# Performance work log

Hardware: AMD Instinct MI355X
Metric: run time of the kernel (lower is better)

Reference implementation:

```python
import jax, jax.numpy as jnp
import numpy as np

N = 50000      # num_nodes
E = 400000     # num_edges
ND = 128       # node_dim (== hidden_dim of GraphNetwork)
HID = 128      # per-head hidden dim in GAT layer
HEADS = 4      # GAT default num_heads
L = 3          # num_layers


def setup_inputs() -> dict:
    key = jax.random.key(0)
    ks = jax.random.split(key, 12)
    s = lambda k, shape, fan: (jax.random.normal(k, shape, jnp.float32) / np.sqrt(fan)).astype(jnp.float32)
    return dict(
        node_features=jax.random.normal(ks[0], (N, ND), jnp.float32),
        edge_index=jax.random.randint(ks[1], (2, E), 0, N, dtype=jnp.int32),
        enc_w1=s(ks[2], (ND, HID), ND), enc_b1=jnp.zeros((HID,), jnp.float32),
        enc_w2=s(ks[3], (HID, HID), HID), enc_b2=jnp.zeros((HID,), jnp.float32),
        gat_W=s(ks[4], (L, HID, HEADS * HID), HID),
        gat_a_src=s(ks[5], (L, HEADS, HID), HID),
        gat_a_dst=s(ks[6], (L, HEADS, HID), HID),
        gat_out_w=s(ks[7], (L, HEADS * HID, HID), HEADS * HID),
        gat_out_b=jnp.zeros((L, HID), jnp.float32),
        out_w1=s(ks[8], (HID, HID), HID), out_b1=jnp.zeros((HID,), jnp.float32),
        out_w2=s(ks[9], (HID, HID), HID), out_b2=jnp.zeros((HID,), jnp.float32),
    )


def _gat_layer(x, row, col, W, a_src, a_dst, ow, ob):
    """One GraphAttentionLayer (eval mode: dropout disabled)."""
    n = x.shape[0]
    h = (x @ W).reshape(n, HEADS, HID)                       # [N,H,D]
    # per-node attention logits (equivalent to (h[row]*a_src).sum(-1) gathered)
    s_src = jnp.einsum('nhd,hd->nh', h, a_src)               # [N,H]
    s_dst = jnp.einsum('nhd,hd->nh', h, a_dst)               # [N,H]
    e = s_src[row] + s_dst[col]                              # [E,H]
    e = jnp.where(e > 0, e, 0.2 * e)                         # LeakyReLU(0.2)
    e_exp = jnp.exp(e)                                       # matches torch: raw exp, no max-shift
    e_sum = jax.ops.segment_sum(e_exp, col, num_segments=n)  # [N,H]
    alpha = e_exp / (e_sum[col] + 1e-8)                      # [E,H]
    msg = h[row] * alpha[:, :, None]                         # [E,H,D]
    out = jax.ops.segment_sum(msg, col, num_segments=n)      # [N,H,D]
    out = out.reshape(n, HEADS * HID) @ ow + ob              # out_proj
    return x + out                                           # residual


def reference(node_features, edge_index, enc_w1, enc_b1, enc_w2, enc_b2,
              gat_W, gat_a_src, gat_a_dst, gat_out_w, gat_out_b,
              out_w1, out_b1, out_w2, out_b2):
    row, col = edge_index[0], edge_index[1]
    # node encoder: Linear-ReLU-Linear
    h = jax.nn.relu(node_features @ enc_w1 + enc_b1) @ enc_w2 + enc_b2
    for i in range(L):
        h = _gat_layer(h, row, col, gat_W[i], gat_a_src[i], gat_a_dst[i],
                       gat_out_w[i], gat_out_b[i])
    # output MLP: Linear-ReLU-Linear
    h = jax.nn.relu(h @ out_w1 + out_b1) @ out_w2 + out_b2
    # batch is None, global_pooling='mean'
    graph_embedding = h.mean(axis=0, keepdims=True)          # [1,HID]
    return h, graph_embedding
```

## Files before the change

### kernel.cpp

```cpp
#include <hip/hip_runtime.h>
#include <math.h>

typedef unsigned short ushort_t;
typedef __attribute__((ext_vector_type(8))) unsigned short ushortx8;
typedef __attribute__((ext_vector_type(4))) unsigned short ushortx4;
typedef __attribute__((ext_vector_type(4))) float floatx4;
typedef __attribute__((ext_vector_type(8))) short frag8;

__device__ __forceinline__ float bf2f(ushort_t u){
  union {unsigned int i; float f;} v; v.i = ((unsigned int)u)<<16; return v.f;
}
__device__ __forceinline__ ushort_t f2bf(float f){
  union {float f; unsigned int i;} v; v.f = f;
  unsigned int x = v.i;
  unsigned int r = x + 0x7fffu + ((x>>16)&1u);
  return (ushort_t)(r>>16);
}

__device__ __forceinline__ void gload16(const void* g, void* l){
  __builtin_amdgcn_global_load_lds(
      (const __attribute__((address_space(1))) unsigned int*)g,
      (__attribute__((address_space(3))) unsigned int*)l, 16, 0, 0);
}

__global__ __launch_bounds__(256) void k_count(const int* __restrict__ col, int* __restrict__ cnt, int E){
  int e = blockIdx.x*256 + threadIdx.x;
  if (e < E) atomicAdd(&cnt[col[e]], 1);
}

__global__ __launch_bounds__(256) void k_scan1(const int* __restrict__ cnt, int* __restrict__ offs,
                                               int* __restrict__ partials, int n){
  __shared__ int buf[256];
  int tid = threadIdx.x;
  int gid = blockIdx.x*256 + tid;
  int v = (gid < n) ? cnt[gid] : 0;
  buf[tid] = v; __syncthreads();
  #pragma unroll
  for (int off=1; off<256; off<<=1){
    int t = (tid >= off) ? buf[tid-off] : 0;
    __syncthreads();
    buf[tid] += t;
    __syncthreads();
  }
  if (gid < n) offs[gid] = buf[tid] - v;
  if (tid == 255) partials[blockIdx.x] = buf[255];
}

__global__ __launch_bounds__(256) void k_scan2(int* __restrict__ partials, int nb){
  __shared__ int buf[256];
  int tid = threadIdx.x;
  int v = (tid < nb) ? partials[tid] : 0;
  buf[tid] = v; __syncthreads();
  #pragma unroll
  for (int off=1; off<256; off<<=1){
    int t = (tid >= off) ? buf[tid-off] : 0;
    __syncthreads();
    buf[tid] += t;
    __syncthreads();
  }
  partials[tid] = buf[tid] - v;
}

__global__ __launch_bounds__(256) void k_scan3(int* __restrict__ offs, const int* __restrict__ partials,
                                               int n, int E){
  int gid = blockIdx.x*256 + threadIdx.x;
  if (gid < n) offs[gid] += partials[blockIdx.x];
  if (blockIdx.x == 0 && threadIdx.x == 0) offs[n] = E;
}

__global__ __launch_bounds__(256) void k_fill(const int* __restrict__ row, const int* __restrict__ col,
                                              const int* __restrict__ offs, int* __restrict__ fill,
                                              int* __restrict__ rowS, int E){
  int e = blockIdx.x*256 + threadIdx.x;
  if (e >= E) return;
  int c = col[e];
  int pos = offs[c] + atomicAdd(&fill[c], 1);
  rowS[pos] = row[e];
}

__global__ __launch_bounds__(256) void k_conv4(const float* __restrict__ src, ushort_t* __restrict__ dst, int n4){
  int i = blockIdx.x*256 + threadIdx.x;
  if (i >= n4) return;
  floatx4 v = ((const floatx4*)src)[i];
  ushortx4 o;
  #pragma unroll
  for (int j=0;j<4;j++) o[j] = f2bf(v[j]);
  ((ushortx4*)dst)[i] = o;
}

template<int K, int NC, int CNT>
__global__ __launch_bounds__(256) void k_convT_b(const float* __restrict__ src, ushort_t* __restrict__ dst){
  int idx = blockIdx.x*256 + threadIdx.x;
  if (idx >= CNT*K*NC) return;
  int l = idx / (K*NC);
  int rem = idx - l*(K*NC);
  int k = rem / NC, n = rem - k*NC;
  dst[(size_t)l*K*NC + (size_t)n*K + k] = f2bf(src[idx]);
}

__global__ __launch_bounds__(256) void k_convT4(const float* __restrict__ s0, const float* __restrict__ s1,
                                                const float* __restrict__ s2, const float* __restrict__ s3,
                                                ushort_t* __restrict__ d0, ushort_t* __restrict__ d1,
                                                ushort_t* __restrict__ d2, ushort_t* __restrict__ d3){
  int idx = blockIdx.x*256 + threadIdx.x;
  if (idx >= 4*16384) return;
  int which = idx >> 14;
  int rem = idx & 16383;
  int k = rem >> 7, n = rem & 127;
  const float* s = which==0 ? s0 : which==1 ? s1 : which==2 ? s2 : s3;
  ushort_t*    d = which==0 ? d0 : which==1 ? d1 : which==2 ? d2 : d3;
  d[n*128 + k] = f2bf(s[rem]);
}

template<bool RELU, bool BIAS, bool RESID, int OMODE, bool SDST, bool COLSUM>
__global__ __launch_bounds__(256) void mfma_gemm(
    const ushort_t* __restrict__ A, const ushort_t* __restrict__ BT,
    const float* __restrict__ bias, const float* __restrict__ resid,
    float* __restrict__ Cf, ushort_t* __restrict__ Cb,
    const float* __restrict__ avec_s, const float* __restrict__ avec_d,
    float* __restrict__ s_src, float* __restrict__ s_dst,
    float* __restrict__ colpart,
    int M, int K, int NC)
{
  __shared__ ushort_t As[128*64];
  __shared__ ushort_t Bs[128*64];
  const int tid  = threadIdx.x;
  const int wid  = tid >> 6, lane = tid & 63;
  const int bm   = blockIdx.y * 128, bn = blockIdx.x * 128;
  const int wr   = (wid >> 1) * 64, wc = (wid & 1) * 64;
  const int lm   = lane & 15;
  const int lk   = (lane >> 4) * 8;

  floatx4 acc[4][4];
  #pragma unroll
  for (int i=0;i<4;i++)
    #pragma unroll
    for (int j=0;j<4;j++) acc[i][j] = floatx4{0.f,0.f,0.f,0.f};

  for (int kc = 0; kc < K; kc += 64){
    #pragma unroll
    for (int i = 0; i < 4; i++){
      int chunk = wid*256 + i*64 + lane;
      int r  = chunk >> 3;
      int c8 = chunk & 7;
      int gr = bm + r; if (gr >= M) gr = M - 1;
      gload16(A  + (size_t)gr*K + kc + c8*8, (char*)As + (size_t)chunk*16);
      gload16(BT + (size_t)(bn + r)*K + kc + c8*8, (char*)Bs + (size_t)chunk*16);
    }
    __syncthreads();

    #pragma unroll
    for (int ks = 0; ks < 2; ks++){
      frag8 a[4], b[4];
      #pragma unroll
      for (int mi=0;mi<4;mi++)
        a[mi] = *(const frag8*)&As[(wr + mi*16 + lm)*64 + ks*32 + lk];
      #pragma unroll
      for (int ni=0;ni<4;ni++)
        b[ni] = *(const frag8*)&Bs[(wc + ni*16 + lm)*64 + ks*32 + lk];
      #pragma unroll
      for (int mi=0;mi<4;mi++)
        #pragma unroll
        for (int ni=0;ni<4;ni++)
          acc[mi][ni] = __builtin_amdgcn_mfma_f32_16x16x32_bf16(a[mi], b[ni], acc[mi][ni], 0, 0, 0);
    }
    __syncthreads();
  }

  const int lr4 = (lane >> 4) * 4;

  float csum[4];
  #pragma unroll
  for (int i=0;i<4;i++) csum[i] = 0.f;

  #pragma unroll
  for (int mi=0;mi<4;mi++){
    #pragma unroll
    for (int ni=0;ni<4;ni++){
      int colg = bn + wc + ni*16 + lm;
      #pragma unroll
      for (int r=0;r<4;r++){
        int rowg = bm + wr + mi*16 + lr4 + r;
        if (rowg < M){
          float v = acc[mi][ni][r];
          if (BIAS)  v += bias[colg];
          if (RELU)  v = v > 0.f ? v : 0.f;
          if (RESID) v += resid[(size_t)rowg*NC + colg];
          if (OMODE == 0 || OMODE == 2) Cf[(size_t)rowg*NC + colg] = v;
          if (OMODE == 1 || OMODE == 2) Cb[(size_t)rowg*NC + colg] = f2bf(v);
          if (COLSUM) csum[ni] += v;
        }
      }
    }
  }

  if constexpr (COLSUM){
    float* sred = (float*)As;
    #pragma unroll
    for (int ni=0;ni<4;ni++){
      float cs = csum[ni];
      cs += __shfl_xor(cs, 16);
      cs += __shfl_xor(cs, 32);
      if (lane < 16)
        sred[(wid>>1)*128 + wc + ni*16 + lane] = cs;
    }
    __syncthreads();
    if (tid < 128)
      colpart[(size_t)blockIdx.y*128 + tid] = sred[tid] + sred[128 + tid];
  }

  if constexpr (SDST){
    const int head = blockIdx.x;
    float* sred = (float*)As;
    float avs[4], avd[4];
    #pragma unroll
    for (int ni=0;ni<4;ni++){
      int d = wc + ni*16 + lm;
      avs[ni] = avec_s[head*128 + d];
      avd[ni] = avec_d[head*128 + d];
    }
    float pss[4][4], psd[4][4];
    #pragma unroll
    for (int mi=0;mi<4;mi++){
      #pragma unroll
      for (int r=0;r<4;r++){
        float vs = 0.f, vd = 0.f;
        #pragma unroll
        for (int ni=0;ni<4;ni++){
          float v = acc[mi][ni][r];
          vs += v * avs[ni];
          vd += v * avd[ni];
        }
        #pragma unroll
        for (int m=1;m<16;m<<=1){
          vs += __shfl_xor(vs, m);
          vd += __shfl_xor(vd, m);
        }
        pss[mi][r] = vs; psd[mi][r] = vd;
      }
    }
    if (lm == 0){
      #pragma unroll
      for (int mi=0;mi<4;mi++)
        #pragma unroll
        for (int r=0;r<4;r++){
          int rl = wr + mi*16 + lr4 + r;
          sred[0*256 + (wid&1)*128 + rl] = pss[mi][r];
          sred[1*256 + (wid&1)*128 + rl] = psd[mi][r];
        }
    }
    __syncthreads();
    int sd = tid >> 7, rl = tid & 127;
    float v = sred[sd*256 + rl] + sred[sd*256 + 128 + rl];
    int rowg = bm + rl;
    if (rowg < M){
      (sd ? s_dst : s_src)[(size_t)rowg*4 + head] = v;
    }
  }
}

__global__ __launch_bounds__(256) void k_gather(const ushort_t* __restrict__ h,
    const float* __restrict__ s_src, const float* __restrict__ s_dst,
    const int* __restrict__ offs, const int* __restrict__ rowS,
    ushort_t* __restrict__ msg, int N)
{
  int wid = threadIdx.x >> 6, lane = threadIdx.x & 63;
  int n = blockIdx.x*4 + wid;
  if (n >= N) return;
  int beg = offs[n], end = offs[n+1];
  const int sub  = lane & 15;
  const int head = lane >> 4;
  const float sdv = s_dst[(size_t)n*4 + head];
  const int c0 = lane*8;

  float acc[8];
  #pragma unroll
  for (int k=0;k<8;k++) acc[k] = 0.f;
  float dsum = 0.f;

  for (int chunk = beg; chunk < end; chunk += 16){
    int m = end - chunk; if (m > 16) m = 16;
    int q = chunk + (sub < m ? sub : m-1);
    int r_p = rowS[q];
    float ss = s_src[(size_t)r_p*4 + head];
    float e = ss + sdv;
    e = e > 0.f ? e : 0.2f*e;
    float w = __expf(e);
    if (sub >= m) w = 0.f;
    dsum += w;

    int j = 0;
    for (; j+1 < m; j += 2){
      int r0 = __shfl(r_p, j);
      int r1 = __shfl(r_p, j+1);
      float w0 = __shfl(w, head*16 + j);
      float w1 = __shfl(w, head*16 + j+1);
      ushortx8 h0 = *(const ushortx8*)(h + (size_t)r0*512 + c0);
      ushortx8 h1 = *(const ushortx8*)(h + (size_t)r1*512 + c0);
      #pragma unroll
      for (int k=0;k<8;k++) acc[k] += w0 * bf2f(h0[k]);
      #pragma unroll
      for (int k=0;k<8;k++) acc[k] += w1 * bf2f(h1[k]);
    }
    if (j < m){
      int r0 = __shfl(r_p, j);
      float w0 = __shfl(w, head*16 + j);
      ushortx8 h0 = *(const ushortx8*)(h + (size_t)r0*512 + c0);
      #pragma unroll
      for (int k=0;k<8;k++) acc[k] += w0 * bf2f(h0[k]);
    }
  }

  float d = dsum;
  #pragma unroll
  for (int mask=1; mask<16; mask<<=1) d += __shfl_xor(d, mask);
  float invd = 1.0f / (d + 1e-8f);

  ushortx8 o;
  #pragma unroll
  for (int k=0;k<8;k++) o[k] = f2bf(acc[k]*invd);
  *(ushortx8*)(msg + (size_t)n*512 + c0) = o;
}

__global__ __launch_bounds__(256) void k_csum2(const float* __restrict__ part, float* __restrict__ out,
                                               int nb, int N){
  __shared__ float buf[256];
  int c = threadIdx.x & 127, half = threadIdx.x >> 7;
  float s = 0.f;
  for (int b = half; b < nb; b += 2) s += part[(size_t)b*128 + c];
  buf[threadIdx.x] = s; __syncthreads();
  if (threadIdx.x < 128) out[c] = (buf[c] + buf[128 + c]) / (float)N;
}

extern "C" void kernel_launch(void* const* d_in, const int* in_sizes, int n_in,
                              void* d_out, int out_size, void* d_ws, size_t ws_size,
                              hipStream_t stream)
{
  const int N = in_sizes[0] / 128;
  const int E = in_sizes[1] / 2;

  const float* nodef  = (const float*)d_in[0];
  const int*   row    = (const int*)d_in[1];
  const int*   col    = row + E;
  const float* enc_w1 = (const float*)d_in[2];
  const float* enc_b1 = (const float*)d_in[3];
  const float* enc_w2 = (const float*)d_in[4];
  const float* enc_b2 = (const float*)d_in[5];
  const float* gat_W  = (const float*)d_in[6];
  const float* a_src  = (const float*)d_in[7];
  const float* a_dst  = (const float*)d_in[8];
  const float* out_w  = (const float*)d_in[9];
  const float* out_b  = (const float*)d_in[10];
  const float* w1     = (const float*)d_in[11];
  const float* b1     = (const float*)d_in[12];
  const float* w2     = (const float*)d_in[13];
  const float* b2     = (const float*)d_in[14];

  char* p = (char*)d_ws;
  auto alloc = [&](size_t bytes)->char*{
    char* r = p; p += (bytes + 255) & ~(size_t)255; return r;
  };
  float*    x     = (float*)   alloc((size_t)N*128*4);
  char*     msgb  =            alloc((size_t)N*512*2);
  ushort_t* h     = (ushort_t*)alloc((size_t)N*512*2);
  ushort_t* xb    = (ushort_t*)alloc((size_t)N*128*2);
  float*    s_src = (float*)   alloc((size_t)N*4*4);
  float*    s_dst = (float*)   alloc((size_t)N*4*4);
  int*      offs  = (int*)     alloc(((size_t)N+1)*4);
  int*      rowS  = (int*)     alloc((size_t)E*4);
  int*      cnt   = (int*)     alloc((size_t)N*4);
  int*      fill  = (int*)     alloc((size_t)N*4);
  int*      parts = (int*)     alloc(1024);
  float*    cpart = (float*)   alloc((size_t)((N+127)/128)*128*4);
  ushort_t* wt_e1 = (ushort_t*)alloc(16384*2);
  ushort_t* wt_e2 = (ushort_t*)alloc(16384*2);
  ushort_t* wt_W  = (ushort_t*)alloc((size_t)3*65536*2);
  ushort_t* wt_o  = (ushort_t*)alloc((size_t)3*65536*2);
  ushort_t* wt_m1 = (ushort_t*)alloc(16384*2);
  ushort_t* wt_m2 = (ushort_t*)alloc(16384*2);

  ushort_t* nfb = h;
  ushort_t* t1  = (ushort_t*)msgb;
  ushort_t* msg = (ushort_t*)msgb;

  hipMemsetAsync(cnt, 0, (size_t)N*4, stream);
  hipMemsetAsync(fill, 0, (size_t)N*4, stream);

  const int gE = (E + 255)/256;
  const int gN = (N + 255)/256;
  const int gW = (N + 3)/4;
  const int gy = (N + 127)/128;
  dim3 blk(256);

  k_count<<<gE, blk, 0, stream>>>(col, cnt, E);
  k_scan1<<<gN, blk, 0, stream>>>(cnt, offs, parts, N);
  k_scan2<<<1,  blk, 0, stream>>>(parts, gN);
  k_scan3<<<gN, blk, 0, stream>>>(offs, parts, N, E);
  k_fill <<<gE, blk, 0, stream>>>(row, col, offs, fill, rowS, E);

  k_convT4<<<(4*16384+255)/256, blk, 0, stream>>>(enc_w1, enc_w2, w1, w2, wt_e1, wt_e2, wt_m1, wt_m2);
  k_convT_b<128,512,3><<<(3*65536+255)/256, blk, 0, stream>>>(gat_W, wt_W);
  k_convT_b<512,128,3><<<(3*65536+255)/256, blk, 0, stream>>>(out_w, wt_o);

  k_conv4<<<(N*128/4 + 255)/256, blk, 0, stream>>>(nodef, nfb, N*128/4);

  mfma_gemm<true ,true ,false,1,false,false><<<dim3(1,gy), blk, 0, stream>>>(nfb, wt_e1, enc_b1, nullptr, nullptr, t1, nullptr, nullptr, nullptr, nullptr, nullptr, N, 128, 128);
  mfma_gemm<false,true ,false,2,false,false><<<dim3(1,gy), blk, 0, stream>>>(t1,  wt_e2, enc_b2, nullptr, x, xb, nullptr, nullptr, nullptr, nullptr, nullptr, N, 128, 128);

  for (int l = 0; l < 3; l++){
    const ushort_t* WT  = wt_W + (size_t)l*65536;
    const ushort_t* OT  = wt_o + (size_t)l*65536;
    const float*    asl = a_src + (size_t)l*512;
    const float*    adl = a_dst + (size_t)l*512;
    const float*    obl = out_b + (size_t)l*128;

    mfma_gemm<false,false,false,1,true,false><<<dim3(4,gy), blk, 0, stream>>>(xb, WT, nullptr, nullptr, nullptr, h, asl, adl, s_src, s_dst, nullptr, N, 128, 512);
    k_gather<<<gW, blk, 0, stream>>>(h, s_src, s_dst, offs, rowS, msg, N);
    mfma_gemm<false,true ,true ,2,false,false><<<dim3(1,gy), blk, 0, stream>>>(msg, OT, obl, x, x, xb, nullptr, nullptr, nullptr, nullptr, nullptr, N, 512, 128);
  }

  mfma_gemm<true ,true ,false,1,false,false><<<dim3(1,gy), blk, 0, stream>>>(xb, wt_m1, b1, nullptr, nullptr, t1, nullptr, nullptr, nullptr, nullptr, nullptr, N, 128, 128);
  mfma_gemm<false,true ,false,0,false,true ><<<dim3(1,gy), blk, 0, stream>>>(t1, wt_m2, b2, nullptr, (float*)d_out, nullptr, nullptr, nullptr, nullptr, nullptr, cpart, N, 128, 128);
  k_csum2<<<1, blk, 0, stream>>>(cpart, (float*)d_out + (size_t)N*128, gy, N);
}
```

Measured before the change: 594.4 us.

## Fuse GEMM chains per row block into encoder, mid-layer and tail kernels

Replaces the separate generic GEMM launches with three fused kernels that keep a 128-row tile in LDS across consecutive GEMMs. The encoder MLP plus the first layer's head projection, each out-projection plus residual plus the next layer's head projection, and the last out-projection plus output MLP plus column sums now each run in one kernel. This removes the bf16 intermediate round trips (t1, xb) and the separate input conversion kernel, and cuts launch count. In exchange the grid for the head projection shrinks from 4×gy to gy blocks, LDS use grows to about 64KB per block, which lowers occupancy, and the four head GEMMs run serially within each block.

Measured after the change: 538.6 us. -9.4%, faster.

```diff
diff --git a/kernel.cpp b/kernel.cpp
--- a/kernel.cpp
+++ b/kernel.cpp
@@ -76,16 +76,6 @@
   int c = col[e];
   int pos = offs[c] + atomicAdd(&fill[c], 1);
   rowS[pos] = row[e];
-}
-
-__global__ __launch_bounds__(256) void k_conv4(const float* __restrict__ src, ushort_t* __restrict__ dst, int n4){
-  int i = blockIdx.x*256 + threadIdx.x;
-  if (i >= n4) return;
-  floatx4 v = ((const floatx4*)src)[i];
-  ushortx4 o;
-  #pragma unroll
-  for (int j=0;j<4;j++) o[j] = f2bf(v[j]);
-  ((ushortx4*)dst)[i] = o;
 }
 
 template<int K, int NC, int CNT>
@@ -112,151 +102,329 @@
   d[n*128 + k] = f2bf(s[rem]);
 }
 
-template<bool RELU, bool BIAS, bool RESID, int OMODE, bool SDST, bool COLSUM>
-__global__ __launch_bounds__(256) void mfma_gemm(
-    const ushort_t* __restrict__ A, const ushort_t* __restrict__ BT,
-    const float* __restrict__ bias, const float* __restrict__ resid,
-    float* __restrict__ Cf, ushort_t* __restrict__ Cb,
-    const float* __restrict__ avec_s, const float* __restrict__ avec_d,
-    float* __restrict__ s_src, float* __restrict__ s_dst,
-    float* __restrict__ colpart,
-    int M, int K, int NC)
+__device__ __forceinline__ void stage_tile64(const ushort_t* src, int ld, int row0, int M, int kc,
+                                             ushort_t* lds, int tid){
+  int wid = tid>>6, lane = tid&63;
+  #pragma unroll
+  for (int i=0;i<4;i++){
+    int chunk = wid*256 + i*64 + lane;
+    int r = chunk>>3, c8 = chunk&7;
+    int gr = row0 + r; if (gr >= M) gr = M-1;
+    gload16(src + (size_t)gr*ld + kc + c8*8, (char*)lds + (size_t)chunk*16);
+  }
+}
+__device__ __forceinline__ void stage_w128(const ushort_t* src, ushort_t* lds, int tid){
+  #pragma unroll
+  for (int i=0;i<8;i++){
+    int chunk = tid + 256*i;
+    gload16(src + (size_t)chunk*8, (char*)lds + (size_t)chunk*16);
+  }
+}
+
+template<int SA,int SB,int NKS>
+__device__ __forceinline__ void ldsgemm(const ushort_t* LA, const ushort_t* LB,
+                                        floatx4 (&acc)[4][4], int wr,int wc,int lm,int lk){
+  #pragma unroll
+  for (int ks=0; ks<NKS; ks++){
+    frag8 a[4], b[4];
+    #pragma unroll
+    for (int mi=0;mi<4;mi++) a[mi] = *(const frag8*)&LA[(wr+mi*16+lm)*SA + ks*32 + lk];
+    #pragma unroll
+    for (int ni=0;ni<4;ni++) b[ni] = *(const frag8*)&LB[(wc+ni*16+lm)*SB + ks*32 + lk];
+    #pragma unroll
+    for (int mi=0;mi<4;mi++)
+      #pragma unroll
+      for (int ni=0;ni<4;ni++)
+        acc[mi][ni] = __builtin_amdgcn_mfma_f32_16x16x32_bf16(a[mi], b[ni], acc[mi][ni], 0, 0, 0);
+  }
+}
+
+__device__ __forceinline__ void zero_acc(floatx4 (&acc)[4][4]){
+  #pragma unroll
+  for (int i=0;i<4;i++)
+    #pragma unroll
+    for (int j=0;j<4;j++) acc[i][j] = floatx4{0.f,0.f,0.f,0.f};
+}
+
+__device__ __forceinline__ void sdst_block(const floatx4 (&acc)[4][4],
+    const float* avec_s, const float* avec_d, float* s_src, float* s_dst, float* sred,
+    int head, int bm, int M, int tid, int wid, int lane, int wr, int wc, int lm, int lr4){
+  float avs[4], avd[4];
+  #pragma unroll
+  for (int ni=0;ni<4;ni++){
+    int d = wc + ni*16 + lm;
+    avs[ni] = avec_s[head*128 + d];
+    avd[ni] = avec_d[head*128 + d];
+  }
+  float pss[4][4], psd[4][4];
+  #pragma unroll
+  for (int mi=0;mi<4;mi++){
+    #pragma unroll
+    for (int r=0;r<4;r++){
+      float vs = 0.f, vd = 0.f;
+      #pragma unroll
+      for (int ni=0;ni<4;ni++){
+        float v = acc[mi][ni][r];
+        vs += v * avs[ni];
+        vd += v * avd[ni];
+      }
+      #pragma unroll
+      for (int m=1;m<16;m<<=1){
+        vs += __shfl_xor(vs, m);
+        vd += __shfl_xor(vd, m);
+      }
+      pss[mi][r] = vs; psd[mi][r] = vd;
+    }
+  }
+  if (lm == 0){
+    #pragma unroll
+    for (int mi=0;mi<4;mi++)
+      #pragma unroll
+      for (int r=0;r<4;r++){
+        int rl = wr + mi*16 + lr4 + r;
+        sred[0*256 + (wid&1)*128 + rl] = pss[mi][r];
+        sred[1*256 + (wid&1)*128 + rl] = psd[mi][r];
+      }
+  }
+  __syncthreads();
+  int sd = tid >> 7, rl = tid & 127;
+  float v = sred[sd*256 + rl] + sred[sd*256 + 128 + rl];
+  int rowg = bm + rl;
+  if (rowg < M) (sd ? s_dst : s_src)[(size_t)rowg*4 + head] = v;
+}
+
+__device__ __forceinline__ void wgemm_heads(const ushort_t* LA_xb, ushort_t* LB,
+    const ushort_t* WT, const float* avs, const float* avd,
+    ushort_t* h, float* s_src, float* s_dst, float* sred,
+    int bm, int M, int tid, int wid, int lane, int wr, int wc, int lm, int lk, int lr4){
+  for (int hb=0; hb<4; hb++){
+    __syncthreads();
+    stage_w128(WT + (size_t)hb*16384, LB, tid);
+    __syncthreads();
+    floatx4 acc[4][4]; zero_acc(acc);
+    ldsgemm<128,128,4>(LA_xb, LB, acc, wr, wc, lm, lk);
+    #pragma unroll
+    for (int mi=0;mi<4;mi++){
+      #pragma unroll
+      for (int ni=0;ni<4;ni++){
+        int colg = wc + ni*16 + lm;
+        #pragma unroll
+        for (int r=0;r<4;r++){
+          int rowg = bm + wr + mi*16 + lr4 + r;
+          if (rowg < M) h[(size_t)rowg*512 + hb*128 + colg] = f2bf(acc[mi][ni][r]);
+        }
+      }
+    }
+    sdst_block(acc, avs, avd, s_src, s_dst, sred, hb, bm, M, tid, wid, lane, wr, wc, lm, lr4);
+  }
+}
+
+__global__ __launch_bounds__(256) void k_enc(
+    const float* __restrict__ nodef,
+    const ushort_t* __restrict__ e1T, const float* __restrict__ eb1,
+    const ushort_t* __restrict__ e2T, const float* __restrict__ eb2,
+    const ushort_t* __restrict__ WT, const float* __restrict__ avs, const float* __restrict__ avd,
+    float* __restrict__ x, ushort_t* __restrict__ h,
+    float* __restrict__ s_src, float* __restrict__ s_dst, int M)
 {
-  __shared__ ushort_t As[128*64];
-  __shared__ ushort_t Bs[128*64];
-  const int tid  = threadIdx.x;
-  const int wid  = tid >> 6, lane = tid & 63;
-  const int bm   = blockIdx.y * 128, bn = blockIdx.x * 128;
-  const int wr   = (wid >> 1) * 64, wc = (wid & 1) * 64;
-  const int lm   = lane & 15;
-  const int lk   = (lane >> 4) * 8;
-
-  floatx4 acc[4][4];
-  #pragma unroll
-  for (int i=0;i<4;i++)
-    #pragma unroll
-    for (int j=0;j<4;j++) acc[i][j] = floatx4{0.f,0.f,0.f,0.f};
-
-  for (int kc = 0; kc < K; kc += 64){
-    #pragma unroll
-    for (int i = 0; i < 4; i++){
-      int chunk = wid*256 + i*64 + lane;
-      int r  = chunk >> 3;
-      int c8 = chunk & 7;
-      int gr = bm + r; if (gr >= M) gr = M - 1;
-      gload16(A  + (size_t)gr*K + kc + c8*8, (char*)As + (size_t)chunk*16);
-      gload16(BT + (size_t)(bn + r)*K + kc + c8*8, (char*)Bs + (size_t)chunk*16);
-    }
-    __syncthreads();
-
-    #pragma unroll
-    for (int ks = 0; ks < 2; ks++){
-      frag8 a[4], b[4];
-      #pragma unroll
-      for (int mi=0;mi<4;mi++)
-        a[mi] = *(const frag8*)&As[(wr + mi*16 + lm)*64 + ks*32 + lk];
-      #pragma unroll
-      for (int ni=0;ni<4;ni++)
-        b[ni] = *(const frag8*)&Bs[(wc + ni*16 + lm)*64 + ks*32 + lk];
-      #pragma unroll
-      for (int mi=0;mi<4;mi++)
-        #pragma unroll
-        for (int ni=0;ni<4;ni++)
-          acc[mi][ni] = __builtin_amdgcn_mfma_f32_16x16x32_bf16(a[mi], b[ni], acc[mi][ni], 0, 0, 0);
-    }
-    __syncthreads();
-  }
-
-  const int lr4 = (lane >> 4) * 4;
+  __shared__ ushort_t LA[128*128];
+  __shared__ ushort_t LB[128*128];
+  __shared__ float sred[512];
+  const int tid = threadIdx.x, wid = tid>>6, lane = tid&63;
+  const int bm = blockIdx.x*128;
+  const int wr = (wid>>1)*64, wc = (wid&1)*64, lm = lane&15, lk = (lane>>4)*8, lr4 = (lane>>4)*4;
+
+  #pragma unroll
+  for (int i=0;i<8;i++){
+    int chunk = tid + 256*i;
+    int r = chunk>>4, c8 = chunk&15;
+    int gr = bm + r; if (gr >= M) gr = M-1;
+    floatx4 lo = *(const floatx4*)(nodef + (size_t)gr*128 + c8*8);
+    floatx4 hi = *(const floatx4*)(nodef + (size_t)gr*128 + c8*8 + 4);
+    ushortx8 v;
+    #pragma unroll
+    for (int j=0;j<4;j++){ v[j] = f2bf(lo[j]); v[j+4] = f2bf(hi[j]); }
+    *(ushortx8*)&LA[r*128 + c8*8] = v;
+  }
+  stage_w128(e1T, LB, tid);
+  __syncthreads();
+
+  floatx4 acc[4][4]; zero_acc(acc);
+  ldsgemm<128,128,4>(LA, LB, acc, wr, wc, lm, lk);
+  __syncthreads();
+  #pragma unroll
+  for (int mi=0;mi<4;mi++)
+    #pragma unroll
+    for (int ni=0;ni<4;ni++){
+      int cl = wc + ni*16 + lm;
+      float b = eb1[cl];
+      #pragma unroll
+      for (int r=0;r<4;r++){
+        float v = acc[mi][ni][r] + b;
+        v = v > 0.f ? v : 0.f;
+        LA[(wr + mi*16 + lr4 + r)*128 + cl] = f2bf(v);
+      }
+    }
+  stage_w128(e2T, LB, tid);
+  __syncthreads();
+
+  zero_acc(acc);
+  ldsgemm<128,128,4>(LA, LB, acc, wr, wc, lm, lk);
+  __syncthreads();
+  #pragma unroll
+  for (int mi=0;mi<4;mi++)
+    #pragma unroll
+    for (int ni=0;ni<4;ni++){
+      int cl = wc + ni*16 + lm;
+      float b = eb2[cl];
+      #pragma unroll
+      for (int r=0;r<4;r++){
+        int rl = wr + mi*16 + lr4 + r;
+        int rowg = bm + rl;
+        float v = acc[mi][ni][r] + b;
+        if (rowg < M) x[(size_t)rowg*128 + cl] = v;
+        LA[rl*128 + cl] = f2bf(v);
+      }
+    }
+
+  wgemm_heads(LA, LB, WT, avs, avd, h, s_src, s_dst, sred,
+              bm, M, tid, wid, lane, wr, wc, lm, lk, lr4);
+}
+
+__global__ __launch_bounds__(256) void k_mid(
+    const ushort_t* __restrict__ msg, const ushort_t* __restrict__ OT, const float* __restrict__ ob,
+    const ushort_t* __restrict__ WT, const float* __restrict__ avs, const float* __restrict__ avd,
+    float* __restrict__ x, ushort_t* __restrict__ h,
+    float* __restrict__ s_src, float* __restrict__ s_dst, int M)
+{
+  __shared__ ushort_t LA[128*128];
+  __shared__ ushort_t LB[128*128];
+  __shared__ float sred[512];
+  const int tid = threadIdx.x, wid = tid>>6, lane = tid&63;
+  const int bm = blockIdx.x*128;
+  const int wr = (wid>>1)*64, wc = (wid&1)*64, lm = lane&15, lk = (lane>>4)*8, lr4 = (lane>>4)*4;
+
+  floatx4 acc[4][4]; zero_acc(acc);
+  for (int kc = 0; kc < 512; kc += 64){
+    stage_tile64(msg, 512, bm, M, kc, LA, tid);
+    stage_tile64(OT,  512, 0, 128, kc, LB, tid);
+    __syncthreads();
+    ldsgemm<64,64,2>(LA, LB, acc, wr, wc, lm, lk);
+    __syncthreads();
+  }
+  #pragma unroll
+  for (int mi=0;mi<4;mi++)
+    #pragma unroll
+    for (int ni=0;ni<4;ni++){
+      int cl = wc + ni*16 + lm;
+      float b = ob[cl];
+      #pragma unroll
+      for (int r=0;r<4;r++){
+        int rl = wr + mi*16 + lr4 + r;
+        int rowg = bm + rl;
+        float v = acc[mi][ni][r] + b;
+        if (rowg < M){
+          v += x[(size_t)rowg*128 + cl];
+          x[(size_t)rowg*128 + cl] = v;
+        }
+        LA[rl*128 + cl] = f2bf(v);
+      }
+    }
+
+  wgemm_heads(LA, LB, WT, avs, avd, h, s_src, s_dst, sred,
+              bm, M, tid, wid, lane, wr, wc, lm, lk, lr4);
+}
+
+__global__ __launch_bounds__(256) void k_tail(
+    const ushort_t* __restrict__ msg, const ushort_t* __restrict__ OT, const float* __restrict__ ob,
+    const ushort_t* __restrict__ m1T, const float* __restrict__ mb1,
+    const ushort_t* __restrict__ m2T, const float* __restrict__ mb2,
+    const float* __restrict__ x, float* __restrict__ out, float* __restrict__ cpart, int M)
+{
+  __shared__ ushort_t LA[128*128];
+  __shared__ ushort_t LB[128*128];
+  __shared__ float sredc[256];
+  const int tid = threadIdx.x, wid = tid>>6, lane = tid&63;
+  const int bm = blockIdx.x*128;
+  const int wr = (wid>>1)*64, wc = (wid&1)*64, lm = lane&15, lk = (lane>>4)*8, lr4 = (lane>>4)*4;
+
+  floatx4 acc[4][4]; zero_acc(acc);
+  for (int kc = 0; kc < 512; kc += 64){
+    stage_tile64(msg, 512, bm, M, kc, LA, tid);
+    stage_tile64(OT,  512, 0, 128, kc, LB, tid);
+    __syncthreads();
+    ldsgemm<64,64,2>(LA, LB, acc, wr, wc, lm, lk);
+    __syncthreads();
+  }
+  #pragma unroll
+  for (int mi=0;mi<4;mi++)
+    #pragma unroll
+    for (int ni=0;ni<4;ni++){
+      int cl = wc + ni*16 + lm;
+      float b = ob[cl];
+      #pragma unroll
+      for (int r=0;r<4;r++){
+        int rl = wr + mi*16 + lr4 + r;
+        int rowg = bm + rl;
+        float v = acc[mi][ni][r] + b;
+        if (rowg < M) v += x[(size_t)rowg*128 + cl];
+        LA[rl*128 + cl] = f2bf(v);
+      }
+    }
+  stage_w128(m1T, LB, tid);
+  __syncthreads();
+
+  zero_acc(acc);
+  ldsgemm<128,128,4>(LA, LB, acc, wr, wc, lm, lk);
+  __syncthreads();
+  #pragma unroll
+  for (int mi=0;mi<4;mi++)
+    #pragma unroll
+    for (int ni=0;ni<4;ni++){
+      int cl = wc + ni*16 + lm;
+      float b = mb1[cl];
+      #pragma unroll
+      for (int r=0;r<4;r++){
+        float v = acc[mi][ni][r] + b;
+        v = v > 0.f ? v : 0.f;
+        LA[(wr + mi*16 + lr4 + r)*128 + cl] = f2bf(v);
+      }
+    }
+  stage_w128(m2T, LB, tid);
+  __syncthreads();
+
+  zero_acc(acc);
+  ldsgemm<128,128,4>(LA, LB, acc, wr, wc, lm, lk);
 
   float csum[4];
   #pragma unroll
   for (int i=0;i<4;i++) csum[i] = 0.f;
-
-  #pragma unroll
-  for (int mi=0;mi<4;mi++){
+  #pragma unroll
+  for (int mi=0;mi<4;mi++)
     #pragma unroll
     for (int ni=0;ni<4;ni++){
-      int colg = bn + wc + ni*16 + lm;
+      int cl = wc + ni*16 + lm;
+      float b = mb2[cl];
       #pragma unroll
       for (int r=0;r<4;r++){
         int rowg = bm + wr + mi*16 + lr4 + r;
         if (rowg < M){
-          float v = acc[mi][ni][r];
-          if (BIAS)  v += bias[colg];
-          if (RELU)  v = v > 0.f ? v : 0.f;
-          if (RESID) v += resid[(size_t)rowg*NC + colg];
-          if (OMODE == 0 || OMODE == 2) Cf[(size_t)rowg*NC + colg] = v;
-          if (OMODE == 1 || OMODE == 2) Cb[(size_t)rowg*NC + colg] = f2bf(v);
-          if (COLSUM) csum[ni] += v;
+          float v = acc[mi][ni][r] + b;
+          out[(size_t)rowg*128 + cl] = v;
+          csum[ni] += v;
         }
       }
     }
-  }
-
-  if constexpr (COLSUM){
-    float* sred = (float*)As;
-    #pragma unroll
-    for (int ni=0;ni<4;ni++){
-      float cs = csum[ni];
-      cs += __shfl_xor(cs, 16);
-      cs += __shfl_xor(cs, 32);
-      if (lane < 16)
-        sred[(wid>>1)*128 + wc + ni*16 + lane] = cs;
-    }
-    __syncthreads();
-    if (tid < 128)
-      colpart[(size_t)blockIdx.y*128 + tid] = sred[tid] + sred[128 + tid];
-  }
-
-  if constexpr (SDST){
-    const int head = blockIdx.x;
-    float* sred = (float*)As;
-    float avs[4], avd[4];
-    #pragma unroll
-    for (int ni=0;ni<4;ni++){
-      int d = wc + ni*16 + lm;
-      avs[ni] = avec_s[head*128 + d];
-      avd[ni] = avec_d[head*128 + d];
-    }
-    float pss[4][4], psd[4][4];
-    #pragma unroll
-    for (int mi=0;mi<4;mi++){
-      #pragma unroll
-      for (int r=0;r<4;r++){
-        float vs = 0.f, vd = 0.f;
-        #pragma unroll
-        for (int ni=0;ni<4;ni++){
-          float v = acc[mi][ni][r];
-          vs += v * avs[ni];
-          vd += v * avd[ni];
-        }
-        #pragma unroll
-        for (int m=1;m<16;m<<=1){
-          vs += __shfl_xor(vs, m);
-          vd += __shfl_xor(vd, m);
-        }
-        pss[mi][r] = vs; psd[mi][r] = vd;
-      }
-    }
-    if (lm == 0){
-      #pragma unroll
-      for (int mi=0;mi<4;mi++)
-        #pragma unroll
-        for (int r=0;r<4;r++){
-          int rl = wr + mi*16 + lr4 + r;
-          sred[0*256 + (wid&1)*128 + rl] = pss[mi][r];
-          sred[1*256 + (wid&1)*128 + rl] = psd[mi][r];
-        }
-    }
-    __syncthreads();
-    int sd = tid >> 7, rl = tid & 127;
-    float v = sred[sd*256 + rl] + sred[sd*256 + 128 + rl];
-    int rowg = bm + rl;
-    if (rowg < M){
-      (sd ? s_dst : s_src)[(size_t)rowg*4 + head] = v;
-    }
-  }
+  __syncthreads();
+  #pragma unroll
+  for (int ni=0;ni<4;ni++){
+    float cs = csum[ni];
+    cs += __shfl_xor(cs, 16);
+    cs += __shfl_xor(cs, 32);
+    if (lane < 16) sredc[(wid>>1)*128 + wc + ni*16 + lane] = cs;
+  }
+  __syncthreads();
+  if (tid < 128) cpart[(size_t)blockIdx.x*128 + tid] = sredc[tid] + sredc[128 + tid];
 }
 
 __global__ __launch_bounds__(256) void k_gather(const ushort_t* __restrict__ h,
@@ -361,9 +529,8 @@
     char* r = p; p += (bytes + 255) & ~(size_t)255; return r;
   };
   float*    x     = (float*)   alloc((size_t)N*128*4);
-  char*     msgb  =            alloc((size_t)N*512*2);
+  ushort_t* msg   = (ushort_t*)alloc((size_t)N*512*2);
   ushort_t* h     = (ushort_t*)alloc((size_t)N*512*2);
-  ushort_t* xb    = (ushort_t*)alloc((size_t)N*128*2);
   float*    s_src = (float*)   alloc((size_t)N*4*4);
   float*    s_dst = (float*)   alloc((size_t)N*4*4);
   int*      offs  = (int*)     alloc(((size_t)N+1)*4);
@@ -379,10 +546,6 @@
   ushort_t* wt_m1 = (ushort_t*)alloc(16384*2);
   ushort_t* wt_m2 = (ushort_t*)alloc(16384*2);
 
-  ushort_t* nfb = h;
-  ushort_t* t1  = (ushort_t*)msgb;
-  ushort_t* msg = (ushort_t*)msgb;
-
   hipMemsetAsync(cnt, 0, (size_t)N*4, stream);
   hipMemsetAsync(fill, 0, (size_t)N*4, stream);
 
@@ -402,24 +565,21 @@
   k_convT_b<128,512,3><<<(3*65536+255)/256, blk, 0, stream>>>(gat_W, wt_W);
   k_convT_b<512,128,3><<<(3*65536+255)/256, blk, 0, stream>>>(out_w, wt_o);
 
-  k_conv4<<<(N*128/4 + 255)/256, blk, 0, stream>>>(nodef, nfb, N*128/4);
-
-  mfma_gemm<true ,true ,false,1,false,false><<<dim3(1,gy), blk, 0, stream>>>(nfb, wt_e1, enc_b1, nullptr, nullptr, t1, nullptr, nullptr, nullptr, nullptr, nullptr, N, 128, 128);
-  mfma_gemm<false,true ,false,2,false,false><<<dim3(1,gy), blk, 0, stream>>>(t1,  wt_e2, enc_b2, nullptr, x, xb, nullptr, nullptr, nullptr, nullptr, nullptr, N, 128, 128);
+  k_enc<<<gy, blk, 0, stream>>>(nodef, wt_e1, enc_b1, wt_e2, enc_b2,
+                                wt_W, a_src, a_dst, x, h, s_src, s_dst, N);
 
   for (int l = 0; l < 3; l++){
-    const ushort_t* WT  = wt_W + (size_t)l*65536;
-    const ushort_t* OT  = wt_o + (size_t)l*65536;
-    const float*    asl = a_src + (size_t)l*512;
-    const float*    adl = a_dst + (size_t)l*512;
-    const float*    obl = out_b + (size_t)l*128;
-
-    mfma_gemm<false,false,false,1,true,false><<<dim3(4,gy), blk, 0, stream>>>(xb, WT, nullptr, nullptr, nullptr, h, asl, adl, s_src, s_dst, nullptr, N, 128, 512);
     k_gather<<<gW, blk, 0, stream>>>(h, s_src, s_dst, offs, rowS, msg, N);
-    mfma_gemm<false,true ,true ,2,false,false><<<dim3(1,gy), blk, 0, stream>>>(msg, OT, obl, x, x, xb, nullptr, nullptr, nullptr, nullptr, nullptr, N, 512, 128);
-  }
-
-  mfma_gemm<true ,true ,false,1,false,false><<<dim3(1,gy), blk, 0, stream>>>(xb, wt_m1, b1, nullptr, nullptr, t1, nullptr, nullptr, nullptr, nullptr, nullptr, N, 128, 128);
-  mfma_gemm<false,true ,false,0,false,true ><<<dim3(1,gy), blk, 0, stream>>>(t1, wt_m2, b2, nullptr, (float*)d_out, nullptr, nullptr, nullptr, nullptr, nullptr, cpart, N, 128, 128);
+    if (l < 2){
+      k_mid<<<gy, blk, 0, stream>>>(msg, wt_o + (size_t)l*65536, out_b + (size_t)l*128,
+                                    wt_W + (size_t)(l+1)*65536,
+                                    a_src + (size_t)(l+1)*512, a_dst + (size_t)(l+1)*512,
+                                    x, h, s_src, s_dst, N);
+    } else {
+      k_tail<<<gy, blk, 0, stream>>>(msg, wt_o + (size_t)2*65536, out_b + (size_t)2*128,
+                                     wt_m1, b1, wt_m2, b2,
+                                     x, (float*)d_out, cpart, N);
+    }
+  }
   k_csum2<<<1, blk, 0, stream>>>(cpart, (float*)d_out + (size_t)N*128, gy, N);
 }
```
